# Kernel optimization log

Measured on AMD Instinct MI355X. Metric: run time of the kernel, lower is better.

Reference implementation:

```python
import jax, jax.numpy as jnp
import numpy as np

N, F, T, C = 20000, 4, 12, 256
HID, OUT = 128, 12
ER, E = 30000, 320000


def _gcn_agg(xw, src, dst, w):
    """GCNConv propagation with self-loops (weight 1): D^-1/2 (A+I) D^-1/2 @ xw.
    xw: [N, T, C] pre-projected features; src/dst: [E] int; w: [E] edge weights."""
    n = xw.shape[0]
    deg = jnp.zeros((n,), xw.dtype).at[dst].add(w) + 1.0  # +1 from self-loop
    dinv = jax.lax.rsqrt(deg)
    coef = (dinv[src] * w * dinv[dst])[:, None, None]      # [E,1,1]
    out = jnp.zeros_like(xw).at[dst].add(coef * xw[src])   # scatter-add messages
    return out + (dinv * dinv)[:, None, None] * xw         # self-loop term


def _regional_conv(x, Wc, bc, regs):
    # Shared GCNConv applied to each of the 5 state graphs, outputs summed.
    xw = jnp.einsum("nft,fc->ntc", x, Wc)  # [N, T, C], all periods at once
    out = bc
    for (src, dst, w) in regs:
        out = out + _gcn_agg(xw, src, dst, w)
    return out


def _forward(x, attrs, idxs, Wc_z, bc_z, Wl_z, bl_z, Wc_h, bc_h, Wl_h, bl_h,
             attention, W1, b1, W2, b2):
    regs = [(idx[0], idx[1], w) for idx, w in zip(idxs, attrs)]
    # A3TGCN runs an independent TGCN-GRU step per period from H=None (zeros),
    # then attention-averages over periods. With H=0:
    #   Z = sigmoid(linear_z([conv_z(X_t), 0]))   (hidden half of Wl drops out)
    #   reset gate R multiplies H=0, so it has no effect on the output
    #   H_tilde = tanh(linear_h([conv_h(X_t), 0]));  H_t = (1-Z)*H_tilde
    cz = _regional_conv(x, Wc_z, bc_z, regs)         # [N, T, C]
    Z = jax.nn.sigmoid(cz @ Wl_z[:C] + bl_z)
    ch = _regional_conv(x, Wc_h, bc_h, regs)
    Htilde = jnp.tanh(ch @ Wl_h[:C] + bl_h)
    Ht = (1.0 - Z) * Htilde                          # [N, T, C]
    probs = jax.nn.softmax(attention)                # [T]
    h = jnp.einsum("ntc,t->nc", Ht, probs)           # temporal attention pooling
    y = jax.nn.relu(h)
    y = jax.nn.relu(y @ W1 + b1)
    y = y @ W2 + b2
    return y, h


def setup_inputs():
    key = jax.random.key(0)
    ks = jax.random.split(key, 32)
    s = 0.05
    inp = {
        "x": jax.random.normal(ks[0], (N, F, T), jnp.float32),
        "edge_index": jax.random.randint(ks[1], (2, E), 0, N, jnp.int32),
    }
    regions = ["IA", "KS", "KY", "OH", "WI"]
    for i, nm in enumerate(regions):
        inp[nm + "edge_index"] = jax.random.randint(ks[2 + i], (2, ER), 0, N, jnp.int32)
    for i, nm in enumerate(regions):
        inp[nm + "edge_attr"] = jax.random.uniform(ks[7 + i], (ER,), jnp.float32)
    for gi, g in enumerate(["z", "r", "h"]):
        inp["Wc_" + g] = jax.random.normal(ks[12 + gi], (F, C), jnp.float32) * s
        inp["bc_" + g] = jnp.zeros((C,), jnp.float32)
        inp["Wl_" + g] = jax.random.normal(ks[15 + gi], (2 * C, C), jnp.float32) * s
        inp["bl_" + g] = jnp.zeros((C,), jnp.float32)
    inp["attention"] = jax.random.normal(ks[18], (T,), jnp.float32)
    inp["W1"] = jax.random.normal(ks[19], (C, HID), jnp.float32) * s
    inp["b1"] = jnp.zeros((HID,), jnp.float32)
    inp["W2"] = jax.random.normal(ks[20], (HID, OUT), jnp.float32) * s
    inp["b2"] = jnp.zeros((OUT,), jnp.float32)
    return inp


def reference(x, edge_index, IAedge_index, KSedge_index, KYedge_index, OHedge_index, WIedge_index,
              IAedge_attr, KSedge_attr, KYedge_attr, OHedge_attr, WIedge_attr,
              Wc_z, bc_z, Wl_z, bl_z, Wc_r, bc_r, Wl_r, bl_r, Wc_h, bc_h, Wl_h, bl_h,
              attention, W1, b1, W2, b2):
    # The full-graph edge_index and the reset-gate parameters are carried by the
    # original module but cannot influence the output (regional convs use the 5
    # state graphs; the reset gate multiplies the zero initial hidden state).
    idxs = [IAedge_index, KSedge_index, KYedge_index, OHedge_index, WIedge_index]
    attrs = [IAedge_attr, KSedge_attr, KYedge_attr, OHedge_attr, WIedge_attr]
    return _forward(x, attrs, idxs, Wc_z, bc_z, Wl_z, bl_z, Wc_h, bc_h, Wl_h, bl_h,
                    attention, W1, b1, W2, b2)
```

## Files before the change

kernel.cpp:

```cpp
#include <hip/hip_runtime.h>

constexpr int N    = 20000;
constexpr int T    = 12;
constexpr int C    = 256;
constexpr int HIDN = 128;
constexpr int OUTD = 12;
constexpr int ER   = 30000;
constexpr int NFT  = 48;
constexpr int EDGE_TOT = 5 * ER;
constexpr int CAP      = 32;
constexpr int EB       = 586;

constexpr int WS_DEG    = 0;
constexpr int WS_CNT    = 100000;
constexpr int WS_MV     = 120000;
constexpr int WS_ZEND   = 122576;
constexpr int WS_WP     = 122576;
constexpr int WS_W2T    = 138960;
constexpr int WS_XV     = 140496;
constexpr int WS_BUCKET = 1100496;

constexpr float LOG2E = 1.4426950408889634f;

typedef __attribute__((ext_vector_type(8))) short short8;
typedef __attribute__((ext_vector_type(4))) float floatx4;

#if __has_builtin(__builtin_amdgcn_exp2f)
#define EXP2(x) __builtin_amdgcn_exp2f(x)
#else
#define EXP2(x) exp2f(x)
#endif

__device__ __forceinline__ short f2bf(float f) {
  unsigned u = __float_as_uint(f);
  u = u + 0x7fffu + ((u >> 16) & 1u);
  return (short)(u >> 16);
}

__device__ __forceinline__ void pick_region(
    int r,
    const int* e0, const int* e1, const int* e2, const int* e3, const int* e4,
    const float* a0, const float* a1, const float* a2, const float* a3, const float* a4,
    const int*& ei, const float*& ea) {
  switch (r) {
    case 0: ei = e0; ea = a0; break;
    case 1: ei = e1; ea = a1; break;
    case 2: ei = e2; ea = a2; break;
    case 3: ei = e3; ea = a3; break;
    default: ei = e4; ea = a4; break;
  }
}

__global__ void k_prep_deg(
    const float* __restrict__ Wc_z, const float* __restrict__ bc_z,
    const float* __restrict__ Wl_z, const float* __restrict__ bl_z,
    const float* __restrict__ Wc_h, const float* __restrict__ bc_h,
    const float* __restrict__ Wl_h, const float* __restrict__ bl_h,
    const float* __restrict__ att, const float* __restrict__ W1,
    const float* __restrict__ W2,
    const int* __restrict__ e0, const int* __restrict__ e1,
    const int* __restrict__ e2, const int* __restrict__ e3,
    const int* __restrict__ e4,
    const float* __restrict__ a0, const float* __restrict__ a1,
    const float* __restrict__ a2, const float* __restrict__ a3,
    const float* __restrict__ a4,
    float* __restrict__ Mv, short* __restrict__ Wp, float* __restrict__ W2t,
    float* __restrict__ deg) {
  int b = blockIdx.x, tid = threadIdx.x;
  if (b < 16) {
    int g  = b >> 3;
    int ch = b & 7;
    int k  = tid;
    const float* Wc = g ? Wc_h : Wc_z;
    const float* bc = g ? bc_h : bc_z;
    const float* Wl = g ? Wl_h : Wl_z;
    const float* bl = g ? bl_h : bl_z;
    float scale = g ? 2.0f * LOG2E : LOG2E;
    float m0 = 0.f, m1 = 0.f, m2 = 0.f, m3 = 0.f;
    float v = (ch == 0) ? bl[k] : 0.0f;
    int c0 = ch * 32;
    for (int c = c0; c < c0 + 32; c++) {
      float wl = Wl[c * C + k];
      m0 = fmaf(Wc[0 * C + c], wl, m0);
      m1 = fmaf(Wc[1 * C + c], wl, m1);
      m2 = fmaf(Wc[2 * C + c], wl, m2);
      m3 = fmaf(Wc[3 * C + c], wl, m3);
      v  = fmaf(bc[c], wl, v);
    }
    float* o = Mv + g * (5 * C);
    atomicAdd(&o[0 * C + k], scale * m0);
    atomicAdd(&o[1 * C + k], scale * m1);
    atomicAdd(&o[2 * C + k], scale * m2);
    atomicAdd(&o[3 * C + k], scale * m3);
    atomicAdd(&o[4 * C + k], scale * v);
    return;
  }
  if (b == 16) {
    if (tid < T) {
      float amax = -3.0e38f;
      for (int t = 0; t < T; t++) amax = fmaxf(amax, att[t]);
      float s = 0.f;
      for (int t = 0; t < T; t++) s += __expf(att[t] - amax);
      Mv[10 * C + tid] = __expf(att[tid] - amax) / s;
    }
    return;
  }
  if (b < 152) {
    int idx = (b - 17) * 256 + tid;
    if (idx < 32768) {
      int j    = idx & 7;
      int lane = (idx >> 3) & 63;
      int ch   = (idx >> 9) & 7;
      int kt   = idx >> 12;
      int cin  = ch * 32 + (lane >> 4) * 8 + j;
      int kout = kt * 16 + (lane & 15);
      Wp[idx] = f2bf(W1[cin * HIDN + kout]);
    } else if (idx < 32768 + 1536) {
      int r = idx - 32768;
      int o = r >> 7, k = r & 127;
      W2t[r] = W2[k * OUTD + o];
    }
    return;
  }
  int i = (b - 152) * 256 + tid;
  if (i >= EDGE_TOT) return;
  int r = i / ER;
  int e = i - r * ER;
  const int* ei; const float* ea;
  pick_region(r, e0, e1, e2, e3, e4, a0, a1, a2, a3, a4, ei, ea);
  atomicAdd(&deg[r * N + ei[ER + e]], ea[e]);
}

__global__ void k_fill(const int* __restrict__ e0, const int* __restrict__ e1,
                       const int* __restrict__ e2, const int* __restrict__ e3,
                       const int* __restrict__ e4,
                       const float* __restrict__ a0, const float* __restrict__ a1,
                       const float* __restrict__ a2, const float* __restrict__ a3,
                       const float* __restrict__ a4,
                       const float* __restrict__ deg, int* __restrict__ cnt,
                       int2* __restrict__ bucket) {
  int i = blockIdx.x * blockDim.x + threadIdx.x;
  if (i >= EDGE_TOT) return;
  int r = i / ER;
  int e = i - r * ER;
  const int* ei; const float* ea;
  pick_region(r, e0, e1, e2, e3, e4, a0, a1, a2, a3, a4, ei, ea);
  int src = ei[e];
  int dst = ei[ER + e];
  float cf = rsqrtf(deg[r * N + src] + 1.0f) * ea[e] * rsqrtf(deg[r * N + dst] + 1.0f);
  int slot = atomicAdd(&cnt[dst], 1);
  if (slot < CAP) bucket[dst * CAP + slot] = make_int2(src, __float_as_int(cf));
}

__global__ __launch_bounds__(256) void k_gather(
    const float* __restrict__ x, const float* __restrict__ deg,
    const int* __restrict__ cnt, const int2* __restrict__ bucket,
    float* __restrict__ xv) {
  int wave = threadIdx.x >> 6, lane = threadIdx.x & 63;
  int n = blockIdx.x * 4 + wave;
  int q = lane < NFT ? lane : NFT - 1;
  float s = 0.f;
#pragma unroll
  for (int r = 0; r < 5; r++) s += 1.0f / (deg[r * N + n] + 1.0f);
  float facc = s * x[n * NFT + q];
  int cv = cnt[n];
  if (cv > CAP) cv = CAP;
  int2 mreg = bucket[n * CAP + (lane & (CAP - 1))];
  for (int j = 0; j < cv; j++) {
    int   src = __shfl(mreg.x, j);
    float cf  = __int_as_float(__shfl(mreg.y, j));
    facc = fmaf(cf, x[src * NFT + q], facc);
  }
  if (lane < NFT) xv[n * NFT + q] = facc;
}

__global__ __launch_bounds__(256) void k_gates_mlp(
    const float* __restrict__ xv, const float* __restrict__ Mv,
    const short* __restrict__ Wp, const float* __restrict__ b1,
    const float* __restrict__ W2t, const float* __restrict__ b2,
    float* __restrict__ y_out, float* __restrict__ h_out) {
  __shared__ short hs[16][264];
  __shared__ float y1s[16][132];
  int tid = threadIdx.x;
  int wave = tid >> 6, lane = tid & 63;
  int quad = lane >> 4, col = lane & 15;
  int n0 = blockIdx.x * 16;

  int half = wave & 1;
  int nb   = (wave >> 1) * 8;
  int c0 = half * 128 + (lane << 1);
  const float* Mz = Mv;
  const float* Mh = Mv + 5 * C;
  float mz[4][2], mh[4][2], vz[2], vh[2];
#pragma unroll
  for (int f = 0; f < 4; f++) {
    float2 t1 = *(const float2*)(Mz + f * C + c0);
    mz[f][0] = t1.x; mz[f][1] = t1.y;
    float2 t2 = *(const float2*)(Mh + f * C + c0);
    mh[f][0] = t2.x; mh[f][1] = t2.y;
  }
  {
    float2 t1 = *(const float2*)(Mz + 4 * C + c0);
    vz[0] = t1.x; vz[1] = t1.y;
    float2 t2 = *(const float2*)(Mh + 4 * C + c0);
    vh[0] = t2.x; vh[1] = t2.y;
  }

#pragma unroll
  for (int nl = 0; nl < 8; nl++) {
    int rl = nb + nl;
    int n = n0 + rl;
    const float* xr = xv + n * NFT;
    float acc[2] = {0.f, 0.f};
#pragma unroll
    for (int tb = 0; tb < 3; tb++) {
      float4 xf0 = *(const float4*)(xr + 0 * T + tb * 4);
      float4 xf1 = *(const float4*)(xr + 1 * T + tb * 4);
      float4 xf2 = *(const float4*)(xr + 2 * T + tb * 4);
      float4 xf3 = *(const float4*)(xr + 3 * T + tb * 4);
      float xs0[4] = {xf0.x, xf0.y, xf0.z, xf0.w};
      float xs1[4] = {xf1.x, xf1.y, xf1.z, xf1.w};
      float xs2[4] = {xf2.x, xf2.y, xf2.z, xf2.w};
      float xs3[4] = {xf3.x, xf3.y, xf3.z, xf3.w};
#pragma unroll
      for (int tt = 0; tt < 4; tt++) {
        int t = tb * 4 + tt;
        float p = Mv[10 * C + t];
        float x0 = xs0[tt], x1 = xs1[tt], x2 = xs2[tt], x3 = xs3[tt];
#pragma unroll
        for (int j = 0; j < 2; j++) {
          float az = fmaf(mz[0][j], x0, fmaf(mz[1][j], x1, fmaf(mz[2][j], x2, fmaf(mz[3][j], x3, vz[j]))));
          float ah = fmaf(mh[0][j], x0, fmaf(mh[1][j], x1, fmaf(mh[2][j], x2, fmaf(mh[3][j], x3, vh[j]))));
          float e1 = EXP2(az);
          float e2 = EXP2(ah);
          float den = (1.0f + e1) * (1.0f + e2);
          float rD  = __builtin_amdgcn_rcpf(den);
          float pn  = fmaf(p, e2, -p);
          acc[j] = fmaf(pn, rD, acc[j]);
        }
      }
    }
    float2 o = {acc[0], acc[1]};
    *(float2*)(h_out + n * C + c0) = o;
    unsigned pk = (unsigned short)f2bf(fmaxf(acc[0], 0.f)) |
                  ((unsigned)(unsigned short)f2bf(fmaxf(acc[1], 0.f)) << 16);
    *(unsigned*)&hs[rl][c0] = pk;
  }
  __syncthreads();

  floatx4 acc2[2];
  acc2[0] = {0.f, 0.f, 0.f, 0.f};
  acc2[1] = {0.f, 0.f, 0.f, 0.f};
#pragma unroll
  for (int ch = 0; ch < 8; ch++) {
    short8 a = *(const short8*)&hs[col][ch * 32 + quad * 8];
#pragma unroll
    for (int kk = 0; kk < 2; kk++) {
      short8 b = ((const short8*)Wp)[((wave * 2 + kk) * 8 + ch) * 64 + lane];
      acc2[kk] = __builtin_amdgcn_mfma_f32_16x16x32_bf16(a, b, acc2[kk], 0, 0, 0);
    }
  }
#pragma unroll
  for (int kk = 0; kk < 2; kk++) {
    int kt = wave * 2 + kk;
    float bias = b1[kt * 16 + col];
#pragma unroll
    for (int r = 0; r < 4; r++)
      y1s[quad * 4 + r][kt * 16 + col] = fmaxf(acc2[kk][r] + bias, 0.f);
  }
  __syncthreads();

  if (tid < 16 * OUTD) {
    int nl = tid / OUTD, o = tid - nl * OUTD;
    float sacc = b2[o];
    const float* yr = &y1s[nl][0];
    const float* wr = W2t + o * HIDN;
#pragma unroll 8
    for (int k4 = 0; k4 < 32; k4++) {
      float4 yv = *(const float4*)(yr + 4 * k4);
      float4 wv = *(const float4*)(wr + 4 * k4);
      sacc = fmaf(yv.x, wv.x, fmaf(yv.y, wv.y, fmaf(yv.z, wv.z, fmaf(yv.w, wv.w, sacc))));
    }
    y_out[(n0 + nl) * OUTD + o] = sacc;
  }
}

extern "C" void kernel_launch(void* const* d_in, const int* in_sizes, int n_in,
                              void* d_out, int out_size, void* d_ws, size_t ws_size,
                              hipStream_t stream) {
  const float* x   = (const float*)d_in[0];
  const int* eIA = (const int*)d_in[2];
  const int* eKS = (const int*)d_in[3];
  const int* eKY = (const int*)d_in[4];
  const int* eOH = (const int*)d_in[5];
  const int* eWI = (const int*)d_in[6];
  const float* aIA = (const float*)d_in[7];
  const float* aKS = (const float*)d_in[8];
  const float* aKY = (const float*)d_in[9];
  const float* aOH = (const float*)d_in[10];
  const float* aWI = (const float*)d_in[11];
  const float* Wc_z = (const float*)d_in[12];
  const float* bc_z = (const float*)d_in[13];
  const float* Wl_z = (const float*)d_in[14];
  const float* bl_z = (const float*)d_in[15];
  const float* Wc_h = (const float*)d_in[20];
  const float* bc_h = (const float*)d_in[21];
  const float* Wl_h = (const float*)d_in[22];
  const float* bl_h = (const float*)d_in[23];
  const float* att  = (const float*)d_in[24];
  const float* W1   = (const float*)d_in[25];
  const float* b1   = (const float*)d_in[26];
  const float* W2   = (const float*)d_in[27];
  const float* b2   = (const float*)d_in[28];

  float* ws     = (float*)d_ws;
  float* deg    = ws + WS_DEG;
  int*   cnt    = (int*)(ws + WS_CNT);
  float* Mv     = ws + WS_MV;
  short* Wp     = (short*)(ws + WS_WP);
  float* W2t    = ws + WS_W2T;
  float* xvb    = ws + WS_XV;
  int2*  bucket = (int2*)(ws + WS_BUCKET);

  float* y_out = (float*)d_out;
  float* h_out = y_out + N * OUTD;

  hipMemsetAsync(deg, 0, WS_ZEND * sizeof(float), stream);

  k_prep_deg<<<152 + EB, 256, 0, stream>>>(Wc_z, bc_z, Wl_z, bl_z,
                                           Wc_h, bc_h, Wl_h, bl_h,
                                           att, W1, W2,
                                           eIA, eKS, eKY, eOH, eWI,
                                           aIA, aKS, aKY, aOH, aWI,
                                           Mv, Wp, W2t, deg);
  k_fill<<<EB, 256, 0, stream>>>(eIA, eKS, eKY, eOH, eWI,
                                 aIA, aKS, aKY, aOH, aWI,
                                 deg, cnt, bucket);
  k_gather<<<N / 4, 256, 0, stream>>>(x, deg, cnt, bucket, xvb);
  k_gates_mlp<<<N / 16, 256, 0, stream>>>(xvb, Mv, Wp, b1, W2t, b2, y_out, h_out);
}
```

Baseline: 198.3 us.

## Fuse neighbor gather into gates/MLP kernel via shared-memory staging

Merges the gather kernel into the gates+MLP kernel. Each block aggregates its 16 nodes' 48 features into shared memory, so the intermediate xv buffer is never written to or read back from global memory and one kernel launch is removed. The gate math is also rewritten with two-wide float vectors in the hope the compiler emits packed FMAs. The cost is that each wave now gathers 4 nodes serially before the gate phase, which could add latency inside the fused kernel.

```diff
diff --git a/kernel.cpp b/kernel.cpp
--- a/kernel.cpp
+++ b/kernel.cpp
@@ -17,19 +17,26 @@
 constexpr int WS_ZEND   = 122576;
 constexpr int WS_WP     = 122576;
 constexpr int WS_W2T    = 138960;
-constexpr int WS_XV     = 140496;
-constexpr int WS_BUCKET = 1100496;
+constexpr int WS_BUCKET = 140496;
 
 constexpr float LOG2E = 1.4426950408889634f;
 
 typedef __attribute__((ext_vector_type(8))) short short8;
 typedef __attribute__((ext_vector_type(4))) float floatx4;
+typedef __attribute__((ext_vector_type(2))) float floatx2;
 
 #if __has_builtin(__builtin_amdgcn_exp2f)
 #define EXP2(x) __builtin_amdgcn_exp2f(x)
 #else
 #define EXP2(x) exp2f(x)
 #endif
+
+__device__ __forceinline__ floatx2 pk_fma(floatx2 a, floatx2 b, floatx2 c) {
+  floatx2 r;
+  r.x = fmaf(a.x, b.x, c.x);
+  r.y = fmaf(a.y, b.y, c.y);
+  return r;
+}
 
 __device__ __forceinline__ short f2bf(float f) {
   unsigned u = __float_as_uint(f);
@@ -152,121 +159,128 @@
   if (slot < CAP) bucket[dst * CAP + slot] = make_int2(src, __float_as_int(cf));
 }
 
-__global__ __launch_bounds__(256) void k_gather(
+__global__ __launch_bounds__(256) void k_fused(
     const float* __restrict__ x, const float* __restrict__ deg,
     const int* __restrict__ cnt, const int2* __restrict__ bucket,
-    float* __restrict__ xv) {
-  int wave = threadIdx.x >> 6, lane = threadIdx.x & 63;
-  int n = blockIdx.x * 4 + wave;
-  int q = lane < NFT ? lane : NFT - 1;
-  float s = 0.f;
-#pragma unroll
-  for (int r = 0; r < 5; r++) s += 1.0f / (deg[r * N + n] + 1.0f);
-  float facc = s * x[n * NFT + q];
-  int cv = cnt[n];
-  if (cv > CAP) cv = CAP;
-  int2 mreg = bucket[n * CAP + (lane & (CAP - 1))];
-  for (int j = 0; j < cv; j++) {
-    int   src = __shfl(mreg.x, j);
-    float cf  = __int_as_float(__shfl(mreg.y, j));
-    facc = fmaf(cf, x[src * NFT + q], facc);
-  }
-  if (lane < NFT) xv[n * NFT + q] = facc;
-}
-
-__global__ __launch_bounds__(256) void k_gates_mlp(
-    const float* __restrict__ xv, const float* __restrict__ Mv,
-    const short* __restrict__ Wp, const float* __restrict__ b1,
-    const float* __restrict__ W2t, const float* __restrict__ b2,
+    const float* __restrict__ Mv, const short* __restrict__ Wp,
+    const float* __restrict__ b1, const float* __restrict__ W2t,
+    const float* __restrict__ b2,
     float* __restrict__ y_out, float* __restrict__ h_out) {
+  __shared__ float xs[16][NFT];
   __shared__ short hs[16][264];
   __shared__ float y1s[16][132];
   int tid = threadIdx.x;
   int wave = tid >> 6, lane = tid & 63;
-  int quad = lane >> 4, col = lane & 15;
   int n0 = blockIdx.x * 16;
 
-  int half = wave & 1;
-  int nb   = (wave >> 1) * 8;
-  int c0 = half * 128 + (lane << 1);
-  const float* Mz = Mv;
-  const float* Mh = Mv + 5 * C;
-  float mz[4][2], mh[4][2], vz[2], vh[2];
-#pragma unroll
-  for (int f = 0; f < 4; f++) {
-    float2 t1 = *(const float2*)(Mz + f * C + c0);
-    mz[f][0] = t1.x; mz[f][1] = t1.y;
-    float2 t2 = *(const float2*)(Mh + f * C + c0);
-    mh[f][0] = t2.x; mh[f][1] = t2.y;
-  }
   {
-    float2 t1 = *(const float2*)(Mz + 4 * C + c0);
-    vz[0] = t1.x; vz[1] = t1.y;
-    float2 t2 = *(const float2*)(Mh + 4 * C + c0);
-    vh[0] = t2.x; vh[1] = t2.y;
-  }
-
-#pragma unroll
-  for (int nl = 0; nl < 8; nl++) {
-    int rl = nb + nl;
-    int n = n0 + rl;
-    const float* xr = xv + n * NFT;
-    float acc[2] = {0.f, 0.f};
-#pragma unroll
-    for (int tb = 0; tb < 3; tb++) {
-      float4 xf0 = *(const float4*)(xr + 0 * T + tb * 4);
-      float4 xf1 = *(const float4*)(xr + 1 * T + tb * 4);
-      float4 xf2 = *(const float4*)(xr + 2 * T + tb * 4);
-      float4 xf3 = *(const float4*)(xr + 3 * T + tb * 4);
-      float xs0[4] = {xf0.x, xf0.y, xf0.z, xf0.w};
-      float xs1[4] = {xf1.x, xf1.y, xf1.z, xf1.w};
-      float xs2[4] = {xf2.x, xf2.y, xf2.z, xf2.w};
-      float xs3[4] = {xf3.x, xf3.y, xf3.z, xf3.w};
-#pragma unroll
-      for (int tt = 0; tt < 4; tt++) {
-        int t = tb * 4 + tt;
-        float p = Mv[10 * C + t];
-        float x0 = xs0[tt], x1 = xs1[tt], x2 = xs2[tt], x3 = xs3[tt];
-#pragma unroll
-        for (int j = 0; j < 2; j++) {
-          float az = fmaf(mz[0][j], x0, fmaf(mz[1][j], x1, fmaf(mz[2][j], x2, fmaf(mz[3][j], x3, vz[j]))));
-          float ah = fmaf(mh[0][j], x0, fmaf(mh[1][j], x1, fmaf(mh[2][j], x2, fmaf(mh[3][j], x3, vh[j]))));
-          float e1 = EXP2(az);
-          float e2 = EXP2(ah);
-          float den = (1.0f + e1) * (1.0f + e2);
-          float rD  = __builtin_amdgcn_rcpf(den);
-          float pn  = fmaf(p, e2, -p);
-          acc[j] = fmaf(pn, rD, acc[j]);
+    int q = lane < NFT ? lane : NFT - 1;
+    for (int nl = 0; nl < 4; nl++) {
+      int rl = wave * 4 + nl;
+      int n = n0 + rl;
+      float s = 0.f;
+#pragma unroll
+      for (int r = 0; r < 5; r++) s += 1.0f / (deg[r * N + n] + 1.0f);
+      float facc = s * x[n * NFT + q];
+      int cv = cnt[n];
+      if (cv > CAP) cv = CAP;
+      int2 mreg = bucket[n * CAP + (lane & (CAP - 1))];
+      for (int j = 0; j < cv; j++) {
+        int   src = __shfl(mreg.x, j);
+        float cf  = __int_as_float(__shfl(mreg.y, j));
+        facc = fmaf(cf, x[src * NFT + q], facc);
+      }
+      if (lane < NFT) xs[rl][lane] = facc;
+    }
+  }
+  __syncthreads();
+
+  {
+    int half = wave & 1;
+    int nb   = (wave >> 1) * 8;
+    int c0 = half * 128 + (lane << 1);
+    const float* Mz = Mv;
+    const float* Mh = Mv + 5 * C;
+    floatx2 mz[4], mh[4], vz, vh;
+#pragma unroll
+    for (int f = 0; f < 4; f++) {
+      mz[f] = *(const floatx2*)(Mz + f * C + c0);
+      mh[f] = *(const floatx2*)(Mh + f * C + c0);
+    }
+    vz = *(const floatx2*)(Mz + 4 * C + c0);
+    vh = *(const floatx2*)(Mh + 4 * C + c0);
+
+#pragma unroll
+    for (int nl = 0; nl < 8; nl++) {
+      int rl = nb + nl;
+      int n = n0 + rl;
+      const float* xr = &xs[rl][0];
+      floatx2 acc = {0.f, 0.f};
+#pragma unroll
+      for (int tb = 0; tb < 3; tb++) {
+        float4 xf0 = *(const float4*)(xr + 0 * T + tb * 4);
+        float4 xf1 = *(const float4*)(xr + 1 * T + tb * 4);
+        float4 xf2 = *(const float4*)(xr + 2 * T + tb * 4);
+        float4 xf3 = *(const float4*)(xr + 3 * T + tb * 4);
+        float xs0[4] = {xf0.x, xf0.y, xf0.z, xf0.w};
+        float xs1[4] = {xf1.x, xf1.y, xf1.z, xf1.w};
+        float xs2[4] = {xf2.x, xf2.y, xf2.z, xf2.w};
+        float xs3[4] = {xf3.x, xf3.y, xf3.z, xf3.w};
+#pragma unroll
+        for (int tt = 0; tt < 4; tt++) {
+          int t = tb * 4 + tt;
+          float p = Mv[10 * C + t];
+          floatx2 x0 = {xs0[tt], xs0[tt]};
+          floatx2 x1 = {xs1[tt], xs1[tt]};
+          floatx2 x2 = {xs2[tt], xs2[tt]};
+          floatx2 x3 = {xs3[tt], xs3[tt]};
+          floatx2 az = pk_fma(mz[0], x0, pk_fma(mz[1], x1, pk_fma(mz[2], x2, pk_fma(mz[3], x3, vz))));
+          floatx2 ah = pk_fma(mh[0], x0, pk_fma(mh[1], x1, pk_fma(mh[2], x2, pk_fma(mh[3], x3, vh))));
+          floatx2 e1, e2;
+          e1.x = EXP2(az.x); e1.y = EXP2(az.y);
+          e2.x = EXP2(ah.x); e2.y = EXP2(ah.y);
+          floatx2 one = {1.f, 1.f};
+          floatx2 d1 = e1 + one;
+          floatx2 d2 = e2 + one;
+          floatx2 rD;
+          rD.x = __builtin_amdgcn_rcpf(d1.x * d2.x);
+          rD.y = __builtin_amdgcn_rcpf(d1.y * d2.y);
+          floatx2 pv = {p, p};
+          floatx2 pn = pk_fma(pv, e2, -pv);
+          acc = pk_fma(pn, rD, acc);
         }
       }
-    }
-    float2 o = {acc[0], acc[1]};
-    *(float2*)(h_out + n * C + c0) = o;
-    unsigned pk = (unsigned short)f2bf(fmaxf(acc[0], 0.f)) |
-                  ((unsigned)(unsigned short)f2bf(fmaxf(acc[1], 0.f)) << 16);
-    *(unsigned*)&hs[rl][c0] = pk;
+      float2 o = {acc.x, acc.y};
+      *(float2*)(h_out + n * C + c0) = o;
+      unsigned pk = (unsigned short)f2bf(fmaxf(acc.x, 0.f)) |
+                    ((unsigned)(unsigned short)f2bf(fmaxf(acc.y, 0.f)) << 16);
+      *(unsigned*)&hs[rl][c0] = pk;
+    }
   }
   __syncthreads();
 
-  floatx4 acc2[2];
-  acc2[0] = {0.f, 0.f, 0.f, 0.f};
-  acc2[1] = {0.f, 0.f, 0.f, 0.f};
-#pragma unroll
-  for (int ch = 0; ch < 8; ch++) {
-    short8 a = *(const short8*)&hs[col][ch * 32 + quad * 8];
+  {
+    int quad = lane >> 4, col = lane & 15;
+    floatx4 acc2[2];
+    acc2[0] = {0.f, 0.f, 0.f, 0.f};
+    acc2[1] = {0.f, 0.f, 0.f, 0.f};
+#pragma unroll
+    for (int ch = 0; ch < 8; ch++) {
+      short8 a = *(const short8*)&hs[col][ch * 32 + quad * 8];
+#pragma unroll
+      for (int kk = 0; kk < 2; kk++) {
+        short8 bb = ((const short8*)Wp)[((wave * 2 + kk) * 8 + ch) * 64 + lane];
+        acc2[kk] = __builtin_amdgcn_mfma_f32_16x16x32_bf16(a, bb, acc2[kk], 0, 0, 0);
+      }
+    }
 #pragma unroll
     for (int kk = 0; kk < 2; kk++) {
-      short8 b = ((const short8*)Wp)[((wave * 2 + kk) * 8 + ch) * 64 + lane];
-      acc2[kk] = __builtin_amdgcn_mfma_f32_16x16x32_bf16(a, b, acc2[kk], 0, 0, 0);
-    }
-  }
-#pragma unroll
-  for (int kk = 0; kk < 2; kk++) {
-    int kt = wave * 2 + kk;
-    float bias = b1[kt * 16 + col];
-#pragma unroll
-    for (int r = 0; r < 4; r++)
-      y1s[quad * 4 + r][kt * 16 + col] = fmaxf(acc2[kk][r] + bias, 0.f);
+      int kt = wave * 2 + kk;
+      float bias = b1[kt * 16 + col];
+#pragma unroll
+      for (int r = 0; r < 4; r++)
+        y1s[quad * 4 + r][kt * 16 + col] = fmaxf(acc2[kk][r] + bias, 0.f);
+    }
   }
   __syncthreads();
 
@@ -319,7 +333,6 @@
   float* Mv     = ws + WS_MV;
   short* Wp     = (short*)(ws + WS_WP);
   float* W2t    = ws + WS_W2T;
-  float* xvb    = ws + WS_XV;
   int2*  bucket = (int2*)(ws + WS_BUCKET);
 
   float* y_out = (float*)d_out;
@@ -336,6 +349,6 @@
   k_fill<<<EB, 256, 0, stream>>>(eIA, eKS, eKY, eOH, eWI,
                                  aIA, aKS, aKY, aOH, aWI,
                                  deg, cnt, bucket);
-  k_gather<<<N / 4, 256, 0, stream>>>(x, deg, cnt, bucket, xvb);
-  k_gates_mlp<<<N / 16, 256, 0, stream>>>(xvb, Mv, Wp, b1, W2t, b2, y_out, h_out);
-}
+  k_fused<<<N / 16, 256, 0, stream>>>(x, deg, cnt, bucket, Mv, Wp, b1, W2t, b2,
+                                      y_out, h_out);
+}
```

Measured after the change: 188.5 us. 4.9% less time.
